# Kernel tuning notes

Measured on AMD Instinct MI355X. Metric: run time of the kernel, lower is better.

The kernel has to match this reference:

```python
import jax, jax.numpy as jnp
import numpy as np

B, L, D, T, S, K = 16, 4095, 768, 768, 64, 8
H = T // 2  # per-direction GRU hidden


def setup_inputs() -> dict:
    key = jax.random.key(0)
    ks = jax.random.split(key, 16)
    sc = 0.05
    hidden = jax.random.normal(ks[0], (B, L, D), jnp.float32)
    attn_len = jax.random.randint(ks[1], (B,), L // 2, L).astype(jnp.int32)
    span_start = jax.random.randint(ks[2], (B, S), 0, L - 16).astype(jnp.int32)
    span_len = jax.random.randint(ks[3], (B, S), 1, 9).astype(jnp.int32)
    return dict(
        hidden=hidden,
        W_ih_f=jax.random.normal(ks[4], (3 * H, D)) * sc,
        W_hh_f=jax.random.normal(ks[5], (3 * H, H)) * sc,
        b_ih_f=jax.random.normal(ks[6], (3 * H,)) * sc,
        b_hh_f=jax.random.normal(ks[7], (3 * H,)) * sc,
        W_ih_b=jax.random.normal(ks[8], (3 * H, D)) * sc,
        W_hh_b=jax.random.normal(ks[9], (3 * H, H)) * sc,
        b_ih_b=jax.random.normal(ks[10], (3 * H,)) * sc,
        b_hh_b=jax.random.normal(ks[11], (3 * H,)) * sc,
        W_ctx=jax.random.normal(ks[12], (T, D)) * sc,
        b_ctx=jax.random.normal(ks[13], (T,)) * sc,
        W_find=jax.random.normal(ks[14], (1, 2 * T)) * sc,
        attn_len=attn_len,
        span_start=span_start,
        span_len=span_len,
    )


def _gru_dir(x, W_ih, W_hh, b_ih, b_hh, reverse):
    # x: [B, S, D] -> [B, S, H]; torch GRU gate order: r, z, n
    def step(h, xt):
        gi = xt @ W_ih.T + b_ih            # [B, 3H]
        gh = h @ W_hh.T + b_hh
        ir, iz, inn = jnp.split(gi, 3, axis=-1)
        hr, hz, hn = jnp.split(gh, 3, axis=-1)
        r = jax.nn.sigmoid(ir + hr)
        z = jax.nn.sigmoid(iz + hz)
        n = jnp.tanh(inn + r * hn)
        h_new = (1.0 - z) * n + z * h
        return h_new, h_new
    xs = jnp.swapaxes(x, 0, 1)             # [S, B, D]
    h0 = jnp.zeros((x.shape[0], W_hh.shape[1]), x.dtype)
    _, ys = jax.lax.scan(step, h0, xs, reverse=reverse)
    return jnp.swapaxes(ys, 0, 1)          # [B, S, H]


def reference(hidden, W_ih_f, W_hh_f, b_ih_f, b_hh_f, W_ih_b, W_hh_b, b_ih_b, b_hh_b,
              W_ctx, b_ctx, W_find, attn_len, span_start, span_len):
    pos = jnp.arange(L)
    # --- per-span mean pooling (ragged spans, vectorized via masks) ---
    end = span_start + span_len - 1        # inclusive end, as hidden[start:end+1]
    mask = (pos[None, None, :] >= span_start[..., None]) & (pos[None, None, :] <= end[..., None])
    maskf = mask.astype(hidden.dtype)      # [B, S, L]
    cnt = maskf.sum(-1, keepdims=True)
    span_rep = jnp.einsum('bsl,bld->bsd', maskf, hidden) / cnt   # [B, S, D]
    # --- bidirectional GRU over the span sequence ---
    h_f = _gru_dir(span_rep, W_ih_f, W_hh_f, b_ih_f, b_hh_f, reverse=False)
    h_b = _gru_dir(span_rep, W_ih_b, W_hh_b, b_ih_b, b_hh_b, reverse=True)
    rep_ac = jnp.concatenate([h_f, h_b], axis=-1)                # [B, S, T]
    # --- context: mean over valid tokens excluding the last valid token, then linear ---
    n_ctx = (attn_len - 1).astype(hidden.dtype)                  # [B]
    ctx_mask = (pos[None, :] < (attn_len - 1)[:, None]).astype(hidden.dtype)
    ctx = jnp.einsum('bl,bld->bd', ctx_mask, hidden) / n_ctx[:, None]
    rep_context = ctx @ W_ctx.T + b_ctx                          # [B, T]
    # --- findm attention: concat + linear(no bias) + sigmoid + topk + gather ---
    all_reps = jnp.concatenate([rep_ac, rep_context[:, None, :]], axis=1)  # [B, S+1, T]
    wq, wk = W_find[0, :T], W_find[0, T:]
    # sigmoid(W [q; k]) = sigmoid(q.wq + k.wk)
    score = jax.nn.sigmoid((rep_ac @ wq)[:, :, None] + (all_reps @ wk)[:, None, :])  # [B, S, S+1]
    vals, idx = jax.lax.top_k(score, K)                          # [B, S, K]
    v1 = jnp.take_along_axis(all_reps[:, None, :, :], idx[..., None], axis=2)        # [B, S, K, T]
    return rep_ac, rep_context, v1, vals, idx
```

## Files before the change

kernel.cpp:

```cpp
#include <hip/hip_runtime.h>
#include <hip/hip_bf16.h>
#include <math.h>

#define BB 16
#define LL 4095
#define DD 768
#define TT 768
#define SS 64
#define KK 8
#define HH 384
#define G3 1152
#define NWPD 24

__global__ void span_mean_kernel(const float* __restrict__ hidden,
                                 const int* __restrict__ sstart,
                                 const int* __restrict__ slen,
                                 float* __restrict__ span,
                                 float* __restrict__ ctx) {
    if (blockIdx.x < 48) ctx[blockIdx.x * 256 + threadIdx.x] = 0.0f;
    int bs = blockIdx.x;
    int b = bs >> 6;
    int st = sstart[bs];
    int ln = slen[bs];
    const float4* base = (const float4*)(hidden + ((size_t)b * LL + st) * DD);
    float4* dst = (float4*)(span + (size_t)bs * DD);
    float inv = 1.0f / (float)ln;
    for (int d = threadIdx.x; d < DD / 4; d += 256) {
        float4 acc = make_float4(0.f, 0.f, 0.f, 0.f);
        for (int r = 0; r < ln; ++r) {
            float4 v = base[(size_t)r * (DD / 4) + d];
            acc.x += v.x; acc.y += v.y; acc.z += v.z; acc.w += v.w;
        }
        dst[d] = make_float4(acc.x * inv, acc.y * inv, acc.z * inv, acc.w * inv);
    }
}

__global__ void ctx_accum_kernel(const float* __restrict__ hidden,
                                 const int* __restrict__ attn_len,
                                 float* __restrict__ ctx) {
    int b = blockIdx.x, chunk = blockIdx.y;
    int lim = attn_len[b] - 1;
    int l0 = chunk * 128;
    int l1 = min(l0 + 128, lim);
    if (l0 >= l1) return;
    int t = threadIdx.x;
    const float* base = hidden + (size_t)b * LL * DD;
    float a0 = 0.f, a1 = 0.f, a2 = 0.f;
    for (int l = l0; l < l1; ++l) {
        const float* row = base + (size_t)l * DD;
        a0 += row[t]; a1 += row[t + 256]; a2 += row[t + 512];
    }
    atomicAdd(&ctx[b * DD + t], a0);
    atomicAdd(&ctx[b * DD + t + 256], a1);
    atomicAdd(&ctx[b * DD + t + 512], a2);
}

__global__ __launch_bounds__(256) void fused_b_kernel(
        const float* __restrict__ span,
        const float* __restrict__ Wf, const float* __restrict__ Wb,
        const float* __restrict__ bihf, const float* __restrict__ bhhf,
        const float* __restrict__ bihb, const float* __restrict__ bhhb,
        float* __restrict__ gi,
        const float* __restrict__ ctxsum, const int* __restrict__ attn_len,
        const float* __restrict__ W_ctx, const float* __restrict__ b_ctx,
        float* __restrict__ out_rc,
        unsigned long long* __restrict__ hpair) {
    int bid = blockIdx.x;
    int t = threadIdx.x;
    if (bid < 576) {
        int mb = bid & 15, nb = (bid >> 4) % 18, dir = bid / 288;
        const float* W = dir ? Wb : Wf;
        const float* bih = dir ? bihb : bihf;
        const float* bhh = dir ? bhhb : bhhf;
        int m0 = mb * 64, n0 = nb * 64;
        __shared__ float As[16][68];
        __shared__ float Bs[16][68];
        int tx = t & 15, ty = t >> 4;
        float acc[4][4] = {{0.f}};
        for (int k0 = 0; k0 < DD; k0 += 16) {
            for (int e = t; e < 1024; e += 256) {
                int r = e >> 4, c = e & 15;
                As[c][r] = span[(size_t)(m0 + r) * DD + k0 + c];
                Bs[c][r] = W[(size_t)(n0 + r) * DD + k0 + c];
            }
            __syncthreads();
#pragma unroll
            for (int kk = 0; kk < 16; ++kk) {
                float4 a4 = *(const float4*)&As[kk][ty * 4];
                float4 b4 = *(const float4*)&Bs[kk][tx * 4];
                float a[4] = {a4.x, a4.y, a4.z, a4.w};
                float bv[4] = {b4.x, b4.y, b4.z, b4.w};
#pragma unroll
                for (int i = 0; i < 4; ++i)
#pragma unroll
                    for (int j = 0; j < 4; ++j) acc[i][j] += a[i] * bv[j];
            }
            __syncthreads();
        }
#pragma unroll
        for (int i = 0; i < 4; ++i)
#pragma unroll
            for (int j = 0; j < 4; ++j) {
                int m = m0 + ty * 4 + i, n = n0 + tx * 4 + j;
                float v = acc[i][j] + bih[n] + (n < 2 * HH ? bhh[n] : 0.0f);
                gi[((size_t)dir * 1024 + m) * G3 + n] = v;
            }
    } else {
        int rb = bid - 576;
        int gid = rb * 256 + t;
        hpair[gid] = 0ull;
        hpair[gid + 12288] = 0ull;
        int b = rb & 15;
        int j = (rb >> 4) * 256 + t;
        __shared__ float cv[DD];
        float inv = 1.0f / (float)(attn_len[b] - 1);
        for (int d = t; d < DD; d += 256) cv[d] = ctxsum[b * DD + d] * inv;
        __syncthreads();
        const float* wr = W_ctx + (size_t)j * DD;
        float acc = b_ctx[j];
        for (int d = 0; d < DD; ++d) acc += wr[d] * cv[d];
        out_rc[b * TT + j] = acc;
    }
}

__global__ __launch_bounds__(256, 1) void scan_coop_kernel(
        const float* __restrict__ gi,
        const float* __restrict__ Whf, const float* __restrict__ Whb,
        const float* __restrict__ bhhf, const float* __restrict__ bhhb,
        unsigned long long* __restrict__ hpair,
        float* __restrict__ repac) {
    int wg = blockIdx.x;
    int dir = wg / NWPD;
    int w = wg % NWPD;
    int t = threadIdx.x;
    int kseg = t & 15, i_loc = t >> 4;
    int i_glob = w * 16 + i_loc;
    const float* Wh = dir ? Whb : Whf;

    float4 wr[3][6];
#pragma unroll
    for (int g = 0; g < 3; ++g)
#pragma unroll
        for (int j = 0; j < 6; ++j) {
            wr[g][j] = *(const float4*)(Wh + (size_t)(g * HH + i_glob) * HH + kseg * 4 + 64 * j);
            asm volatile("" : "+v"(wr[g][j].x), "+v"(wr[g][j].y),
                              "+v"(wr[g][j].z), "+v"(wr[g][j].w));
        }
    float bhn = (dir ? bhhb : bhhf)[2 * HH + i_glob];

    __shared__ __align__(16) float hs[6144];
    float4* hs4 = (float4*)hs;

    for (int s = 0; s < 64; ++s) {
        int p = dir ? (63 - s) : s;
        const float* grow = gi + ((size_t)dir * 1024 + kseg * 64 + p) * G3;
        float g_r = grow[i_glob], g_z = grow[HH + i_glob], g_n = grow[2 * HH + i_glob];
        {
            const unsigned long long* src = hpair + (size_t)((s & 1) * 2 + dir) * 6144;
            unsigned int expect = (unsigned int)s;
            unsigned long long vals[24];
            for (;;) {
#pragma unroll
                for (int j = 0; j < 24; ++j) {
                    unsigned int off = (unsigned int)((j * 256 + t) * 8);
                    asm volatile("global_load_dwordx2 %0, %1, %2 sc0 sc1"
                                 : "=v"(vals[j]) : "v"(off), "s"(src));
                }
                asm volatile("s_waitcnt vmcnt(0)" ::: "memory");
                __builtin_amdgcn_sched_barrier(0);
                bool ok = true;
#pragma unroll
                for (int j = 0; j < 24; ++j) ok &= ((unsigned int)(vals[j] >> 32) == expect);
                if (ok) break;
                __builtin_amdgcn_s_sleep(1);
            }
#pragma unroll
            for (int j = 0; j < 24; ++j)
                hs[j * 256 + t] = __uint_as_float((unsigned int)vals[j]);
        }
        __syncthreads();
        float pr[16], pz[16], pn[16];
#pragma unroll
        for (int b = 0; b < 16; ++b) {
            float4 hq[6];
#pragma unroll
            for (int j = 0; j < 6; ++j) hq[j] = hs4[b * 96 + kseg + 16 * j];
            float ar = 0.f, az = 0.f, an = 0.f;
#pragma unroll
            for (int j = 0; j < 6; ++j) {
                ar += wr[0][j].x * hq[j].x + wr[0][j].y * hq[j].y + wr[0][j].z * hq[j].z + wr[0][j].w * hq[j].w;
                az += wr[1][j].x * hq[j].x + wr[1][j].y * hq[j].y + wr[1][j].z * hq[j].z + wr[1][j].w * hq[j].w;
                an += wr[2][j].x * hq[j].x + wr[2][j].y * hq[j].y + wr[2][j].z * hq[j].z + wr[2][j].w * hq[j].w;
            }
            pr[b] = ar; pz[b] = az; pn[b] = an;
        }
        float qr[8], qz[8], qn[8];
        {
            const bool hi = (kseg & 8) != 0;
#pragma unroll
            for (int j = 0; j < 8; ++j) {
                float sr_ = hi ? pr[j] : pr[j + 8];
                qr[j] = (hi ? pr[j + 8] : pr[j]) + __shfl_xor(sr_, 8);
                float sz_ = hi ? pz[j] : pz[j + 8];
                qz[j] = (hi ? pz[j + 8] : pz[j]) + __shfl_xor(sz_, 8);
                float sn_ = hi ? pn[j] : pn[j + 8];
                qn[j] = (hi ? pn[j + 8] : pn[j]) + __shfl_xor(sn_, 8);
            }
        }
        float ur[4], uz[4], un[4];
        {
            const bool hi = (kseg & 4) != 0;
#pragma unroll
            for (int j = 0; j < 4; ++j) {
                float sr_ = hi ? qr[j] : qr[j + 4];
                ur[j] = (hi ? qr[j + 4] : qr[j]) + __shfl_xor(sr_, 4);
                float sz_ = hi ? qz[j] : qz[j + 4];
                uz[j] = (hi ? qz[j + 4] : qz[j]) + __shfl_xor(sz_, 4);
                float sn_ = hi ? qn[j] : qn[j + 4];
                un[j] = (hi ? qn[j + 4] : qn[j]) + __shfl_xor(sn_, 4);
            }
        }
        float vr[2], vz[2], vn[2];
        {
            const bool hi = (kseg & 2) != 0;
#pragma unroll
            for (int j = 0; j < 2; ++j) {
                float sr_ = hi ? ur[j] : ur[j + 2];
                vr[j] = (hi ? ur[j + 2] : ur[j]) + __shfl_xor(sr_, 2);
                float sz_ = hi ? uz[j] : uz[j + 2];
                vz[j] = (hi ? uz[j + 2] : uz[j]) + __shfl_xor(sz_, 2);
                float sn_ = hi ? un[j] : un[j + 2];
                vn[j] = (hi ? un[j + 2] : un[j]) + __shfl_xor(sn_, 2);
            }
        }
        float sr, sz, sn;
        {
            const bool hi = (kseg & 1) != 0;
            float sr_ = hi ? vr[0] : vr[1];
            sr = (hi ? vr[1] : vr[0]) + __shfl_xor(sr_, 1);
            float sz_ = hi ? vz[0] : vz[1];
            sz = (hi ? vz[1] : vz[0]) + __shfl_xor(sz_, 1);
            float sn_ = hi ? vn[0] : vn[1];
            sn = (hi ? vn[1] : vn[0]) + __shfl_xor(sn_, 1);
        }
        float r = 1.0f / (1.0f + expf(-(g_r + sr)));
        float z = 1.0f / (1.0f + expf(-(g_z + sz)));
        float n = tanhf(g_n + r * (sn + bhn));
        float hold = hs[kseg * 384 + i_glob];
        float hnew = (1.0f - z) * n + z * hold;
        unsigned long long pv = ((unsigned long long)(unsigned int)(s + 1) << 32)
                              | (unsigned long long)__float_as_uint(hnew);
        __hip_atomic_store(hpair + (size_t)(((s + 1) & 1) * 2 + dir) * 6144 + kseg * 384 + i_glob,
                           pv, __ATOMIC_RELAXED, __HIP_MEMORY_SCOPE_AGENT);
        repac[(size_t)(kseg * 64 + p) * TT + dir * HH + i_glob] = hnew;
        asm volatile("s_waitcnt lgkmcnt(0)" ::: "memory");
        __builtin_amdgcn_sched_barrier(0);
        __builtin_amdgcn_s_barrier();
    }
}

__global__ void qkv_kernel(const float* __restrict__ repac,
                           const float* __restrict__ repctx,
                           const float* __restrict__ Wfind,
                           float* __restrict__ qv, float* __restrict__ kv) {
    int w = blockIdx.x * 4 + (threadIdx.x >> 6);
    int lane = threadIdx.x & 63;
    const float* row;
    const float* vec;
    float* dst;
    if (w < 1024) {
        row = repac + (size_t)w * TT;
        vec = Wfind;
        dst = qv + w;
    } else {
        int u = w - 1024;
        int b = u / 65, j = u % 65;
        row = (j < 64) ? (repac + (size_t)(b * 64 + j) * TT) : (repctx + (size_t)b * TT);
        vec = Wfind + TT;
        dst = kv + u;
    }
    double acc = 0.0;
    for (int d = lane; d < TT; d += 64) acc += (double)row[d] * (double)vec[d];
#pragma unroll
    for (int off = 32; off > 0; off >>= 1) acc += __shfl_down(acc, off);
    if (lane == 0) *dst = (float)acc;
}

__global__ __launch_bounds__(64) void topk_kernel(
                            const float* __restrict__ qv,
                            const float* __restrict__ kv,
                            float* __restrict__ vals_out,
                            float* __restrict__ idx_out,
                            int* __restrict__ idxw) {
    int t = threadIdx.x;
    int b = blockIdx.x;
    int bs = b * 64 + t;
    __shared__ float kvs[65];
    for (int e = t; e < 65; e += 64) kvs[e] = kv[b * 65 + e];
    __syncthreads();
    float q = qv[bs];
    float sc[65];
#pragma unroll
    for (int j = 0; j < 65; ++j) {
        float x = q + kvs[j];
        float e = (float)exp(-(double)x);
        sc[j] = 1.0f / (1.0f + e);
    }
    unsigned long long taken = 0ull;
    bool tk64 = false;
    for (int kk = 0; kk < 8; ++kk) {
        float best = -3.0e38f;
        int bj = 0;
#pragma unroll
        for (int j = 0; j < 65; ++j) {
            bool tkn = (j < 64) ? (((taken >> j) & 1ull) != 0ull) : tk64;
            float v = sc[j];
            if (!tkn && v > best) { best = v; bj = j; }
        }
        if (bj < 64) taken |= (1ull << bj); else tk64 = true;
        vals_out[bs * 8 + kk] = best;
        idx_out[bs * 8 + kk] = (float)bj;
        idxw[bs * 8 + kk] = bj;
    }
}

__global__ void v1_kernel(const float* __restrict__ repac,
                          const float* __restrict__ repctx,
                          const int* __restrict__ idxw,
                          float* __restrict__ v1) {
    int bs = blockIdx.x;
    int b = bs >> 6;
    int t = threadIdx.x;
    for (int kk = 0; kk < 8; ++kk) {
        int j = idxw[bs * 8 + kk];
        const float4* src = (const float4*)((j < 64) ? (repac + (size_t)(b * 64 + j) * TT)
                                                     : (repctx + (size_t)b * TT));
        float4* dst = (float4*)(v1 + ((size_t)bs * 8 + kk) * TT);
        for (int d = t; d < DD / 4; d += 256) dst[d] = src[d];
    }
}

extern "C" void kernel_launch(void* const* d_in, const int* in_sizes, int n_in,
                              void* d_out, int out_size, void* d_ws, size_t ws_size,
                              hipStream_t stream) {
    const float* hidden    = (const float*)d_in[0];
    const float* W_ih_f    = (const float*)d_in[1];
    const float* W_hh_f    = (const float*)d_in[2];
    const float* b_ih_f    = (const float*)d_in[3];
    const float* b_hh_f    = (const float*)d_in[4];
    const float* W_ih_b    = (const float*)d_in[5];
    const float* W_hh_b    = (const float*)d_in[6];
    const float* b_ih_b    = (const float*)d_in[7];
    const float* b_hh_b    = (const float*)d_in[8];
    const float* W_ctx     = (const float*)d_in[9];
    const float* b_ctx     = (const float*)d_in[10];
    const float* W_find    = (const float*)d_in[11];
    const int*   attn_len  = (const int*)d_in[12];
    const int*   span_start= (const int*)d_in[13];
    const int*   span_len  = (const int*)d_in[14];
    (void)in_sizes; (void)n_in; (void)out_size; (void)ws_size;

    float* ws   = (float*)d_ws;
    float* span = ws;
    float* gi   = span + 786432;
    float* ctx  = gi + 2359296;
    float* qv   = ctx + 12288;
    float* kv   = qv + 1024;
    int*   idxw = (int*)(kv + 1040);

    float* out      = (float*)d_out;
    float* o_repac  = out;
    float* o_repctx = out + 786432;
    float* o_v1     = out + 798720;
    float* o_vals   = out + 7090176;
    float* o_idx    = out + 7098368;

    unsigned long long* hpair = (unsigned long long*)o_v1;

    span_mean_kernel<<<1024, 256, 0, stream>>>(hidden, span_start, span_len, span, ctx);
    ctx_accum_kernel<<<dim3(BB, 32), 256, 0, stream>>>(hidden, attn_len, ctx);
    fused_b_kernel<<<624, 256, 0, stream>>>(span, W_ih_f, W_ih_b,
                                            b_ih_f, b_hh_f, b_ih_b, b_hh_b, gi,
                                            ctx, attn_len, W_ctx, b_ctx,
                                            o_repctx, hpair);
    scan_coop_kernel<<<48, 256, 0, stream>>>(gi, W_hh_f, W_hh_b, b_hh_f, b_hh_b,
                                             hpair, o_repac);
    qkv_kernel<<<516, 256, 0, stream>>>(o_repac, o_repctx, W_find, qv, kv);
    topk_kernel<<<16, 64, 0, stream>>>(qv, kv, o_vals, o_idx, idxw);
    v1_kernel<<<1024, 256, 0, stream>>>(o_repac, o_repctx, idxw, o_v1);
}
```

Measured before the change: 878.2 us.

## Merge span/context kernels, drop atomics, widen GRU scan workgroups

Merges span-mean and context-accumulation into one launch. Context partial sums now go to per-chunk slots (placed in the v1 output region) rather than atomics, and fused_b sums them. The recurrent scan now uses 12 workgroups of 1024 threads instead of 48 of 256, so fewer blocks have to poll the global h exchange each step, and each thread polls 6 entries instead of 24. The trade-off is larger per-block barriers, plus an unrolled 32-way reduction in the ctx path. Scratch space in the output buffer is reused before v1 overwrites it.

```diff
diff --git a/kernel.cpp b/kernel.cpp
--- a/kernel.cpp
+++ b/kernel.cpp
@@ -10,49 +10,46 @@
 #define KK 8
 #define HH 384
 #define G3 1152
-#define NWPD 24
-
-__global__ void span_mean_kernel(const float* __restrict__ hidden,
-                                 const int* __restrict__ sstart,
-                                 const int* __restrict__ slen,
-                                 float* __restrict__ span,
-                                 float* __restrict__ ctx) {
-    if (blockIdx.x < 48) ctx[blockIdx.x * 256 + threadIdx.x] = 0.0f;
-    int bs = blockIdx.x;
-    int b = bs >> 6;
-    int st = sstart[bs];
-    int ln = slen[bs];
-    const float4* base = (const float4*)(hidden + ((size_t)b * LL + st) * DD);
-    float4* dst = (float4*)(span + (size_t)bs * DD);
-    float inv = 1.0f / (float)ln;
-    for (int d = threadIdx.x; d < DD / 4; d += 256) {
-        float4 acc = make_float4(0.f, 0.f, 0.f, 0.f);
-        for (int r = 0; r < ln; ++r) {
-            float4 v = base[(size_t)r * (DD / 4) + d];
-            acc.x += v.x; acc.y += v.y; acc.z += v.z; acc.w += v.w;
-        }
-        dst[d] = make_float4(acc.x * inv, acc.y * inv, acc.z * inv, acc.w * inv);
-    }
-}
-
-__global__ void ctx_accum_kernel(const float* __restrict__ hidden,
-                                 const int* __restrict__ attn_len,
-                                 float* __restrict__ ctx) {
-    int b = blockIdx.x, chunk = blockIdx.y;
-    int lim = attn_len[b] - 1;
-    int l0 = chunk * 128;
-    int l1 = min(l0 + 128, lim);
-    if (l0 >= l1) return;
-    int t = threadIdx.x;
-    const float* base = hidden + (size_t)b * LL * DD;
-    float a0 = 0.f, a1 = 0.f, a2 = 0.f;
-    for (int l = l0; l < l1; ++l) {
-        const float* row = base + (size_t)l * DD;
-        a0 += row[t]; a1 += row[t + 256]; a2 += row[t + 512];
-    }
-    atomicAdd(&ctx[b * DD + t], a0);
-    atomicAdd(&ctx[b * DD + t + 256], a1);
-    atomicAdd(&ctx[b * DD + t + 512], a2);
+#define NWPD 6
+
+__global__ void spanctx_kernel(const float* __restrict__ hidden,
+                               const int* __restrict__ sstart,
+                               const int* __restrict__ slen,
+                               const int* __restrict__ attn_len,
+                               float* __restrict__ span,
+                               float* __restrict__ ctx_part) {
+    int bid = blockIdx.x;
+    int t = threadIdx.x;
+    if (bid < 1024) {
+        int b = bid >> 6;
+        int st = sstart[bid];
+        int ln = slen[bid];
+        const float4* base = (const float4*)(hidden + ((size_t)b * LL + st) * DD);
+        float4* dst = (float4*)(span + (size_t)bid * DD);
+        float inv = 1.0f / (float)ln;
+        for (int d = t; d < DD / 4; d += 256) {
+            float4 acc = make_float4(0.f, 0.f, 0.f, 0.f);
+            for (int r = 0; r < ln; ++r) {
+                float4 v = base[(size_t)r * (DD / 4) + d];
+                acc.x += v.x; acc.y += v.y; acc.z += v.z; acc.w += v.w;
+            }
+            dst[d] = make_float4(acc.x * inv, acc.y * inv, acc.z * inv, acc.w * inv);
+        }
+    } else {
+        int rb = bid - 1024;
+        int b = rb >> 5, chunk = rb & 31;
+        int lim = attn_len[b] - 1;
+        int l0 = chunk * 128;
+        int l1 = min(l0 + 128, lim);
+        const float* base = hidden + (size_t)b * LL * DD;
+        float a0 = 0.f, a1 = 0.f, a2 = 0.f;
+        for (int l = l0; l < l1; ++l) {
+            const float* row = base + (size_t)l * DD;
+            a0 += row[t]; a1 += row[t + 256]; a2 += row[t + 512];
+        }
+        float* dst = ctx_part + ((size_t)chunk * 16 + b) * DD;
+        dst[t] = a0; dst[t + 256] = a1; dst[t + 512] = a2;
+    }
 }
 
 __global__ __launch_bounds__(256) void fused_b_kernel(
@@ -61,7 +58,7 @@
         const float* __restrict__ bihf, const float* __restrict__ bhhf,
         const float* __restrict__ bihb, const float* __restrict__ bhhb,
         float* __restrict__ gi,
-        const float* __restrict__ ctxsum, const int* __restrict__ attn_len,
+        const float* __restrict__ ctx_part, const int* __restrict__ attn_len,
         const float* __restrict__ W_ctx, const float* __restrict__ b_ctx,
         float* __restrict__ out_rc,
         unsigned long long* __restrict__ hpair) {
@@ -114,7 +111,12 @@
         int j = (rb >> 4) * 256 + t;
         __shared__ float cv[DD];
         float inv = 1.0f / (float)(attn_len[b] - 1);
-        for (int d = t; d < DD; d += 256) cv[d] = ctxsum[b * DD + d] * inv;
+        for (int d = t; d < DD; d += 256) {
+            float s = 0.f;
+            for (int c = 0; c < 32; ++c)
+                s += ctx_part[((size_t)c * 16 + b) * DD + d];
+            cv[d] = s * inv;
+        }
         __syncthreads();
         const float* wr = W_ctx + (size_t)j * DD;
         float acc = b_ctx[j];
@@ -123,7 +125,7 @@
     }
 }
 
-__global__ __launch_bounds__(256, 1) void scan_coop_kernel(
+__global__ __launch_bounds__(1024, 1) void scan_coop_kernel(
         const float* __restrict__ gi,
         const float* __restrict__ Whf, const float* __restrict__ Whb,
         const float* __restrict__ bhhf, const float* __restrict__ bhhb,
@@ -134,7 +136,7 @@
     int w = wg % NWPD;
     int t = threadIdx.x;
     int kseg = t & 15, i_loc = t >> 4;
-    int i_glob = w * 16 + i_loc;
+    int i_glob = w * 64 + i_loc;
     const float* Wh = dir ? Whb : Whf;
 
     float4 wr[3][6];
@@ -158,25 +160,21 @@
         {
             const unsigned long long* src = hpair + (size_t)((s & 1) * 2 + dir) * 6144;
             unsigned int expect = (unsigned int)s;
-            unsigned long long vals[24];
+            unsigned long long vals[6];
             for (;;) {
-#pragma unroll
-                for (int j = 0; j < 24; ++j) {
-                    unsigned int off = (unsigned int)((j * 256 + t) * 8);
-                    asm volatile("global_load_dwordx2 %0, %1, %2 sc0 sc1"
-                                 : "=v"(vals[j]) : "v"(off), "s"(src));
+                bool ok = true;
+#pragma unroll
+                for (int j = 0; j < 6; ++j) {
+                    vals[j] = __hip_atomic_load(src + j * 1024 + t,
+                                                __ATOMIC_RELAXED, __HIP_MEMORY_SCOPE_AGENT);
+                    ok &= ((unsigned int)(vals[j] >> 32) == expect);
                 }
-                asm volatile("s_waitcnt vmcnt(0)" ::: "memory");
-                __builtin_amdgcn_sched_barrier(0);
-                bool ok = true;
-#pragma unroll
-                for (int j = 0; j < 24; ++j) ok &= ((unsigned int)(vals[j] >> 32) == expect);
                 if (ok) break;
                 __builtin_amdgcn_s_sleep(1);
             }
 #pragma unroll
-            for (int j = 0; j < 24; ++j)
-                hs[j * 256 + t] = __uint_as_float((unsigned int)vals[j]);
+            for (int j = 0; j < 6; ++j)
+                hs[j * 1024 + t] = __uint_as_float((unsigned int)vals[j]);
         }
         __syncthreads();
         float pr[16], pz[16], pn[16];
@@ -253,9 +251,7 @@
         __hip_atomic_store(hpair + (size_t)(((s + 1) & 1) * 2 + dir) * 6144 + kseg * 384 + i_glob,
                            pv, __ATOMIC_RELAXED, __HIP_MEMORY_SCOPE_AGENT);
         repac[(size_t)(kseg * 64 + p) * TT + dir * HH + i_glob] = hnew;
-        asm volatile("s_waitcnt lgkmcnt(0)" ::: "memory");
-        __builtin_amdgcn_sched_barrier(0);
-        __builtin_amdgcn_s_barrier();
+        __syncthreads();
     }
 }
 
@@ -363,8 +359,7 @@
     float* ws   = (float*)d_ws;
     float* span = ws;
     float* gi   = span + 786432;
-    float* ctx  = gi + 2359296;
-    float* qv   = ctx + 12288;
+    float* qv   = gi + 2359296;
     float* kv   = qv + 1024;
     int*   idxw = (int*)(kv + 1040);
 
@@ -376,15 +371,16 @@
     float* o_idx    = out + 7098368;
 
     unsigned long long* hpair = (unsigned long long*)o_v1;
-
-    span_mean_kernel<<<1024, 256, 0, stream>>>(hidden, span_start, span_len, span, ctx);
-    ctx_accum_kernel<<<dim3(BB, 32), 256, 0, stream>>>(hidden, attn_len, ctx);
+    float* ctx_part = o_v1 + 49152;
+
+    spanctx_kernel<<<1536, 256, 0, stream>>>(hidden, span_start, span_len, attn_len,
+                                             span, ctx_part);
     fused_b_kernel<<<624, 256, 0, stream>>>(span, W_ih_f, W_ih_b,
                                             b_ih_f, b_hh_f, b_ih_b, b_hh_b, gi,
-                                            ctx, attn_len, W_ctx, b_ctx,
+                                            ctx_part, attn_len, W_ctx, b_ctx,
                                             o_repctx, hpair);
-    scan_coop_kernel<<<48, 256, 0, stream>>>(gi, W_hh_f, W_hh_b, b_hh_f, b_hh_b,
-                                             hpair, o_repac);
+    scan_coop_kernel<<<2 * NWPD, 1024, 0, stream>>>(gi, W_hh_f, W_hh_b, b_hh_f, b_hh_b,
+                                                    hpair, o_repac);
     qkv_kernel<<<516, 256, 0, stream>>>(o_repac, o_repctx, W_find, qv, kv);
     topk_kernel<<<16, 64, 0, stream>>>(qv, kv, o_vals, o_idx, idxw);
     v1_kernel<<<1024, 256, 0, stream>>>(o_repac, o_repctx, idxw, o_v1);
```

New measurement: 1.865 ms. 2.12x slower.
